# Optimization experiments

Measured on AMD Instinct MI355X. Metric: run time of the kernel, lower is better.

The kernel has to match this reference:

```python
import jax, jax.numpy as jnp
import numpy as np

T, WAY, SHOT, QUERY, C = 4, 16, 8, 256, 256

def setup_inputs() -> dict:
    key = jax.random.key(0)
    k1, k2, k3 = jax.random.split(key, 3)
    query_feat = jax.random.normal(k1, (T, WAY * QUERY, C), dtype=jnp.float32)
    support_feat = jax.random.normal(k2, (T, WAY * SHOT, C), dtype=jnp.float32)
    support_target = jax.random.randint(k3, (T, WAY * SHOT), 0, WAY, dtype=jnp.int64)
    return {
        "query_feat": query_feat,
        "support_feat": support_feat,
        "support_target": support_target,
        "way_num": WAY,
        "shot_num": SHOT,
        "query_num": QUERY,
    }

def reference(query_feat, support_feat, support_target, way_num, shot_num, query_num):
    t, wq, c = query_feat.shape
    # prototype = mean over shots: (t, way, shot, c) -> (t, way, c)
    proto_feat = jnp.mean(
        support_feat.reshape(t, way_num, shot_num, c), axis=2
    )
    q = query_feat.reshape(t, way_num * query_num, c)
    # negative squared euclidean distance: (t, wq, way)
    diff = q[:, :, None, :] - proto_feat[:, None, :, :]  # (t, wq, way, c)
    return -jnp.sum(diff * diff, axis=3)
```

## Files before the change

kernel.cpp:

```cpp
#include <hip/hip_runtime.h>


constexpr int T_    = 4;
constexpr int WAY   = 16;
constexpr int SHOT  = 8;
constexpr int QUERY = 256;
constexpr int C     = 256;
constexpr int WQ    = WAY * QUERY;
constexpr int QT    = 32;
constexpr int NTHR  = 128;
constexpr int PAD   = C + 4;

__global__ __launch_bounds__(NTHR) void proto_dist_kernel(
    const float* __restrict__ query,
    const float* __restrict__ support,
    float* __restrict__ out)
{
    __shared__ float ps[WAY][PAD];
    __shared__ float qs[QT][PAD];

    const int tid = threadIdx.x;
    constexpr int BLOCKS_PER_T = WQ / QT;
    const int t  = blockIdx.x / BLOCKS_PER_T;
    const int qb = (blockIdx.x % BLOCKS_PER_T) * QT;

    const float* sup_t = support + (size_t)t * (WAY * SHOT * C);
    for (int c = tid; c < C; c += NTHR) {
        #pragma unroll
        for (int w = 0; w < WAY; ++w) {
            float s = 0.f;
            const float* sw = sup_t + (w * SHOT) * C + c;
            #pragma unroll
            for (int sh = 0; sh < SHOT; ++sh) s += sw[sh * C];
            ps[w][c] = s * (1.0f / SHOT);
        }
    }

    const float4* qsrc = (const float4*)(query + ((size_t)t * WQ + qb) * C);
    #pragma unroll
    for (int i = 0; i < (QT * C / 4) / NTHR; ++i) {
        int idx = tid + i * NTHR;
        int q   = idx / (C / 4);
        int c4  = (idx % (C / 4)) * 4;
        float4 v = qsrc[idx];
        float* dst = &qs[q][c4];
        dst[0] = v.x; dst[1] = v.y; dst[2] = v.z; dst[3] = v.w;
    }
    __syncthreads();

    const int q  = tid >> 2;
    const int wg = (tid & 3) * 4;
    float acc[4] = {0.f, 0.f, 0.f, 0.f};
    #pragma unroll 4
    for (int c = 0; c < C; c += 4) {
        float4 qv = *(const float4*)&qs[q][c];
        #pragma unroll
        for (int j = 0; j < 4; ++j) {
            float4 pv = *(const float4*)&ps[wg + j][c];
            float d0 = qv.x - pv.x;
            float d1 = qv.y - pv.y;
            float d2 = qv.z - pv.z;
            float d3 = qv.w - pv.w;
            acc[j] += d0 * d0 + d1 * d1 + d2 * d2 + d3 * d3;
        }
    }

    float4 r;
    r.x = -acc[0]; r.y = -acc[1]; r.z = -acc[2]; r.w = -acc[3];
    float4* dst = (float4*)(out + (((size_t)t * WQ + qb + q) * WAY + wg));
    *dst = r;
}

extern "C" void kernel_launch(void* const* d_in, const int* in_sizes, int n_in,
                              void* d_out, int out_size, void* d_ws, size_t ws_size,
                              hipStream_t stream) {
    const float* query   = (const float*)d_in[0];
    const float* support = (const float*)d_in[1];
    float* out = (float*)d_out;

    dim3 grid(T_ * (WQ / QT));
    proto_dist_kernel<<<grid, NTHR, 0, stream>>>(query, support, out);
}
```

Baseline: 82.12 us.

## Precompute prototypes in separate kernel and use 2x2 register tiling for distances

Prototype means are computed once per task by a small first kernel into workspace, so the 512 distance blocks no longer each re-read and re-average all support rows. The distance kernel loads the prototypes from workspace, stores shared memory with float4 writes, and gives each thread a 2-query by 2-way tile instead of 1 query by 4 ways, which reuses each shared-memory load more. The cost is a second kernel launch and an extra global round trip for the prototypes.

```diff
diff --git a/kernel.cpp b/kernel.cpp
--- a/kernel.cpp
+++ b/kernel.cpp
@@ -4,71 +4,110 @@
 constexpr int T_    = 4;
 constexpr int WAY   = 16;
 constexpr int SHOT  = 8;
-constexpr int QUERY = 256;
 constexpr int C     = 256;
-constexpr int WQ    = WAY * QUERY;
-constexpr int QT    = 32;
-constexpr int NTHR  = 128;
-constexpr int PAD   = C + 4;
+constexpr int WQ    = 4096;
+constexpr int C4    = C / 4;
+constexpr int PITCH = 260;
 
-__global__ __launch_bounds__(NTHR) void proto_dist_kernel(
+__global__ __launch_bounds__(256) void proto_kernel(
+    const float* __restrict__ support,
+    float* __restrict__ proto)
+{
+    const int t       = blockIdx.x >> 2;
+    const int quarter = blockIdx.x & 3;
+    const int idx     = quarter * 256 + threadIdx.x;
+    const int w  = idx >> 6;
+    const int c4 = idx & 63;
+
+    const float4* row = (const float4*)(support + (size_t)t * (WAY * SHOT * C))
+                        + (w * SHOT) * C4 + c4;
+    float4 s = make_float4(0.f, 0.f, 0.f, 0.f);
+    #pragma unroll
+    for (int sh = 0; sh < SHOT; ++sh) {
+        float4 v = row[sh * C4];
+        s.x += v.x; s.y += v.y; s.z += v.z; s.w += v.w;
+    }
+    s.x *= 0.125f; s.y *= 0.125f; s.z *= 0.125f; s.w *= 0.125f;
+
+    float4* dst = (float4*)(proto + (size_t)t * (WAY * C));
+    dst[w * C4 + c4] = s;
+}
+
+__global__ __launch_bounds__(128) void dist_kernel(
     const float* __restrict__ query,
-    const float* __restrict__ support,
+    const float* __restrict__ proto,
     float* __restrict__ out)
 {
-    __shared__ float ps[WAY][PAD];
-    __shared__ float qs[QT][PAD];
+    __shared__ float ps[WAY * PITCH];
+    __shared__ float qs[32  * PITCH];
 
     const int tid = threadIdx.x;
-    constexpr int BLOCKS_PER_T = WQ / QT;
-    const int t  = blockIdx.x / BLOCKS_PER_T;
-    const int qb = (blockIdx.x % BLOCKS_PER_T) * QT;
+    const int t   = blockIdx.x >> 7;
+    const int qb  = (blockIdx.x & 127) * 32;
 
-    const float* sup_t = support + (size_t)t * (WAY * SHOT * C);
-    for (int c = tid; c < C; c += NTHR) {
+    {
+        const float4* src = (const float4*)(proto + (size_t)t * (WAY * C));
         #pragma unroll
-        for (int w = 0; w < WAY; ++w) {
-            float s = 0.f;
-            const float* sw = sup_t + (w * SHOT) * C + c;
-            #pragma unroll
-            for (int sh = 0; sh < SHOT; ++sh) s += sw[sh * C];
-            ps[w][c] = s * (1.0f / SHOT);
+        for (int i = 0; i < 8; ++i) {
+            int idx = tid + i * 128;
+            int w = idx >> 6, c4 = idx & 63;
+            float4 v = src[idx];
+            *(float4*)&ps[w * PITCH + c4 * 4] = v;
         }
     }
-
-    const float4* qsrc = (const float4*)(query + ((size_t)t * WQ + qb) * C);
-    #pragma unroll
-    for (int i = 0; i < (QT * C / 4) / NTHR; ++i) {
-        int idx = tid + i * NTHR;
-        int q   = idx / (C / 4);
-        int c4  = (idx % (C / 4)) * 4;
-        float4 v = qsrc[idx];
-        float* dst = &qs[q][c4];
-        dst[0] = v.x; dst[1] = v.y; dst[2] = v.z; dst[3] = v.w;
+    {
+        const float4* src = (const float4*)(query + ((size_t)t * WQ + qb) * C);
+        #pragma unroll
+        for (int i = 0; i < 16; ++i) {
+            int idx = tid + i * 128;
+            int q = idx >> 6, c4 = idx & 63;
+            float4 v = src[idx];
+            *(float4*)&qs[q * PITCH + c4 * 4] = v;
+        }
     }
     __syncthreads();
 
-    const int q  = tid >> 2;
-    const int wg = (tid & 3) * 4;
-    float acc[4] = {0.f, 0.f, 0.f, 0.f};
-    #pragma unroll 4
+    const int ql = tid >> 3;
+    const int wg = (tid & 7) * 2;
+
+    const float* q0 = &qs[(2 * ql + 0) * PITCH];
+    const float* q1 = &qs[(2 * ql + 1) * PITCH];
+    const float* p0 = &ps[(wg + 0) * PITCH];
+    const float* p1 = &ps[(wg + 1) * PITCH];
+
+    float a00 = 0.f, a01 = 0.f, a10 = 0.f, a11 = 0.f;
+    #pragma unroll 8
     for (int c = 0; c < C; c += 4) {
-        float4 qv = *(const float4*)&qs[q][c];
-        #pragma unroll
-        for (int j = 0; j < 4; ++j) {
-            float4 pv = *(const float4*)&ps[wg + j][c];
-            float d0 = qv.x - pv.x;
-            float d1 = qv.y - pv.y;
-            float d2 = qv.z - pv.z;
-            float d3 = qv.w - pv.w;
-            acc[j] += d0 * d0 + d1 * d1 + d2 * d2 + d3 * d3;
-        }
+        float4 qa = *(const float4*)(q0 + c);
+        float4 qv = *(const float4*)(q1 + c);
+        float4 pa = *(const float4*)(p0 + c);
+        float4 pb = *(const float4*)(p1 + c);
+
+        float d;
+        d = qa.x - pa.x; a00 += d * d;
+        d = qa.y - pa.y; a00 += d * d;
+        d = qa.z - pa.z; a00 += d * d;
+        d = qa.w - pa.w; a00 += d * d;
+
+        d = qa.x - pb.x; a01 += d * d;
+        d = qa.y - pb.y; a01 += d * d;
+        d = qa.z - pb.z; a01 += d * d;
+        d = qa.w - pb.w; a01 += d * d;
+
+        d = qv.x - pa.x; a10 += d * d;
+        d = qv.y - pa.y; a10 += d * d;
+        d = qv.z - pa.z; a10 += d * d;
+        d = qv.w - pa.w; a10 += d * d;
+
+        d = qv.x - pb.x; a11 += d * d;
+        d = qv.y - pb.y; a11 += d * d;
+        d = qv.z - pb.z; a11 += d * d;
+        d = qv.w - pb.w; a11 += d * d;
     }
 
-    float4 r;
-    r.x = -acc[0]; r.y = -acc[1]; r.z = -acc[2]; r.w = -acc[3];
-    float4* dst = (float4*)(out + (((size_t)t * WQ + qb + q) * WAY + wg));
-    *dst = r;
+    float* ob = out + (((size_t)t * WQ + qb + 2 * ql) * WAY + wg);
+    *(float2*)ob         = make_float2(-a00, -a01);
+    *(float2*)(ob + WAY) = make_float2(-a10, -a11);
 }
 
 extern "C" void kernel_launch(void* const* d_in, const int* in_sizes, int n_in,
@@ -76,8 +115,9 @@
                               hipStream_t stream) {
     const float* query   = (const float*)d_in[0];
     const float* support = (const float*)d_in[1];
-    float* out = (float*)d_out;
+    float* out   = (float*)d_out;
+    float* proto = (float*)d_ws;
 
-    dim3 grid(T_ * (WQ / QT));
-    proto_dist_kernel<<<grid, NTHR, 0, stream>>>(query, support, out);
+    proto_kernel<<<dim3(T_ * 4), 256, 0, stream>>>(support, proto);
+    dist_kernel <<<dim3(T_ * 128), 128, 0, stream>>>(query, proto, out);
 }
```

Result: faster. 79.04 us (-3.7%).
